# Performance work log

Hardware: AMD Instinct MI355X
Metric: run time of the kernel (lower is better)

Reference implementation:

```python
import jax, jax.numpy as jnp
import numpy as np

N = 4  # n_qubits


def _apply_1q(state, gate, q):
    # state: (B, 2**N) complex64; gate: (2,2) or (B,2,2) complex64; wire q (wire 0 = most significant)
    B = state.shape[0]
    left, right = 2 ** q, 2 ** (N - q - 1)
    s = state.reshape(B, left, 2, right)
    if gate.ndim == 3:
        out = jnp.einsum('bij,bajc->baic', gate, s)
    else:
        out = jnp.einsum('ij,bajc->baic', gate, s)
    return out.reshape(B, 2 ** N)


def _cnot(state, q):
    # CNOT control=q, target=q+1: flip target amplitudes where control bit is 1
    B = state.shape[0]
    left, right = 2 ** q, 2 ** (N - q - 2)
    s = state.reshape(B, left, 2, 2, right)
    out = jnp.concatenate([s[:, :, 0:1], s[:, :, 1:2, ::-1, :]], axis=2)
    return out.reshape(B, 2 ** N)


def _circuit(angles, theta):
    # angles: (B, N) float32 data-dependent RY encoding; theta: (L, N, 3) shared params
    B = angles.shape[0]
    state = jnp.zeros((B, 2 ** N), dtype=jnp.complex64).at[:, 0].set(1.0)
    h = angles * 0.5
    c, s = jnp.cos(h), jnp.sin(h)
    for q in range(N):
        ry = jnp.stack([jnp.stack([c[:, q], -s[:, q]], -1),
                        jnp.stack([s[:, q], c[:, q]], -1)], -2).astype(jnp.complex64)  # (B,2,2)
        state = _apply_1q(state, ry, q)
    L = theta.shape[0]
    for l in range(L):
        for q in range(N):
            a = theta[l, q, 0] * 0.5
            b = theta[l, q, 1] * 0.5
            cc = theta[l, q, 2] * 0.5
            ca, sa = jnp.cos(a), jnp.sin(a)
            rx = jnp.stack([jnp.stack([ca + 0j, -1j * sa]),
                            jnp.stack([-1j * sa, ca + 0j])]).astype(jnp.complex64)
            state = _apply_1q(state, rx, q)
            zero = jnp.zeros((), jnp.complex64)
            rz = jnp.stack([jnp.stack([jnp.exp(-1j * b), zero]),
                            jnp.stack([zero, jnp.exp(1j * b)])]).astype(jnp.complex64)
            state = _apply_1q(state, rz, q)
            cy, sy = jnp.cos(cc), jnp.sin(cc)
            ry = jnp.stack([jnp.stack([cy + 0j, -sy + 0j]),
                            jnp.stack([sy + 0j, cy + 0j])]).astype(jnp.complex64)
            state = _apply_1q(state, ry, q)
        for q in range(N - 1):
            state = _cnot(state, q)
    # PauliZ expectation per wire from probabilities
    probs = (state.real ** 2 + state.imag ** 2).reshape((B,) + (2,) * N)
    evs = []
    for q in range(N):
        sign = (1.0 - 2.0 * jnp.arange(2, dtype=jnp.float32)).reshape(
            (1,) * (q + 1) + (2,) + (1,) * (N - q - 1))
        evs.append((probs * sign).sum(axis=tuple(range(1, N + 1))))
    return jnp.stack(evs, axis=-1)  # (B, N)


def setup_inputs() -> dict:
    key = jax.random.key(0)
    ks = jax.random.split(key, 6)
    B, D = 32768, 512
    inputs = jax.random.normal(ks[0], (B, D), dtype=jnp.float32)
    prev_h = jnp.tanh(jax.random.normal(ks[1], (B, N), dtype=jnp.float32))
    W_enc = jax.random.normal(ks[2], (D + N, N), dtype=jnp.float32) * 0.05
    b_enc = jnp.zeros((N,), dtype=jnp.float32)
    theta = jax.random.uniform(ks[3], (2, N, 3), minval=-0.1, maxval=0.1, dtype=jnp.float32)
    W_out = jax.random.normal(ks[4], (N, N), dtype=jnp.float32) * 0.5
    b_out = jnp.zeros((N,), dtype=jnp.float32)
    return {"inputs": inputs, "prev_h": prev_h, "W_enc": W_enc, "b_enc": b_enc,
            "theta": theta, "W_out": W_out, "b_out": b_out}


def reference(inputs, prev_h, W_enc, b_enc, theta, W_out, b_out):
    combined = jnp.concatenate([inputs, prev_h], axis=-1)           # (B, D+N)
    angles = jnp.tanh(combined @ W_enc + b_enc) * jnp.float32(np.pi)  # (B, N)
    expvals = _circuit(angles, theta)                               # (B, N)
    next_h = jnp.tanh(expvals @ W_out + b_out)                      # (B, N)
    return next_h
```

## Files before the change

kernel.cpp:

```cpp
#include <hip/hip_runtime.h>
#include <math.h>

#define DQ 512
#define NQ 4
#define LQ 2
#define RPB 64
#define BLOCK 256

__device__ __forceinline__ float rowsum16(float v) {
    int x;
    x = __builtin_amdgcn_update_dpp(0, __float_as_int(v), 0x121, 0xF, 0xF, true);
    v += __int_as_float(x);
    x = __builtin_amdgcn_update_dpp(0, __float_as_int(v), 0x122, 0xF, 0xF, true);
    v += __int_as_float(x);
    x = __builtin_amdgcn_update_dpp(0, __float_as_int(v), 0x124, 0xF, 0xF, true);
    v += __int_as_float(x);
    x = __builtin_amdgcn_update_dpp(0, __float_as_int(v), 0x128, 0xF, 0xF, true);
    v += __int_as_float(x);
    return v;
}

__global__ __launch_bounds__(BLOCK) void qrnn_kernel(
    const float* __restrict__ inputs,
    const float* __restrict__ prev_h,
    const float* __restrict__ W_enc,
    const float* __restrict__ b_enc,
    const float* __restrict__ theta,
    const float* __restrict__ W_out,
    const float* __restrict__ b_out,
    float* __restrict__ out,
    int B)
{
    __shared__ float4 sPart[RPB][5];
    __shared__ float  sC[RPB * 5];
    __shared__ float  sS[RPB * 5];
    __shared__ float  sU[LQ * NQ * 8];

    const int tid  = threadIdx.x;
    const int lane = tid & 63;
    const int wave = tid >> 6;
    const int blockBase = blockIdx.x * RPB;

    if (tid < LQ * NQ) {
        const int l = tid >> 2, q = tid & 3;
        const float a  = theta[(l * NQ + q) * 3 + 0] * 0.5f;
        const float b  = theta[(l * NQ + q) * 3 + 1] * 0.5f;
        const float cc = theta[(l * NQ + q) * 3 + 2] * 0.5f;
        float sa, ca, sb, cb, sy, cy;
        sincosf(a,  &sa, &ca);
        sincosf(b,  &sb, &cb);
        sincosf(cc, &sy, &cy);
        const float m00r =  ca * cb, m00i = -ca * sb;
        const float m01r = -sa * sb, m01i = -sa * cb;
        const float m10r =  sa * sb, m10i = -sa * cb;
        const float m11r =  ca * cb, m11i =  ca * sb;
        float* u = &sU[tid * 8];
        u[0] = cy * m00r - sy * m10r;  u[1] = cy * m00i - sy * m10i;
        u[2] = cy * m01r - sy * m11r;  u[3] = cy * m01i - sy * m11i;
        u[4] = sy * m00r + cy * m10r;  u[5] = sy * m00i + cy * m10i;
        u[6] = sy * m01r + cy * m11r;  u[7] = sy * m01i + cy * m11i;
    }

    const float4* __restrict__ W4 = (const float4*)W_enc;
    float4 wreg[8];
#pragma unroll
    for (int k = 0; k < 4; ++k) {
        wreg[k]     = W4[4 * lane + k];
        wreg[k + 4] = W4[256 + 4 * lane + k];
    }

    const int r0 = wave * 16;
    const float4* __restrict__ inBase = (const float4*)inputs;

    float4 xb[4][2];
#pragma unroll
    for (int p = 0; p < 4; ++p) {
        const float4* in4 = inBase + (size_t)(blockBase + r0 + p) * (DQ / 4);
        xb[p][0] = in4[lane];
        xb[p][1] = in4[lane + 64];
    }

#pragma unroll
    for (int r = 0; r < 16; ++r) {
        const int slot = r & 3;
        const float4 x0 = xb[slot][0];
        const float4 x1 = xb[slot][1];
        if (r + 4 < 16) {
            const float4* in4 = inBase + (size_t)(blockBase + r0 + r + 4) * (DQ / 4);
            xb[slot][0] = in4[lane];
            xb[slot][1] = in4[lane + 64];
        }

        const float xs[8] = { x0.x, x0.y, x0.z, x0.w, x1.x, x1.y, x1.z, x1.w };
        float4 acc = make_float4(0.f, 0.f, 0.f, 0.f);
#pragma unroll
        for (int k = 0; k < 8; ++k) {
            acc.x += xs[k] * wreg[k].x;
            acc.y += xs[k] * wreg[k].y;
            acc.z += xs[k] * wreg[k].z;
            acc.w += xs[k] * wreg[k].w;
        }
        acc.x = rowsum16(acc.x);
        acc.y = rowsum16(acc.y);
        acc.z = rowsum16(acc.z);
        acc.w = rowsum16(acc.w);
        if ((lane & 15) == 0) sPart[r0 + r][lane >> 4] = acc;
    }

    __syncthreads();

    {
        const int row  = tid >> 2;
        const int comp = tid & 3;
        const float* pp = (const float*)&sPart[row][0];
        float s = pp[0 * 4 + comp] + pp[1 * 4 + comp] + pp[2 * 4 + comp] + pp[3 * 4 + comp];

        const float4 ph = *(const float4*)(prev_h + (size_t)(blockBase + row) * 4);
        s += ph.x * W_enc[512 * 4 + comp];
        s += ph.y * W_enc[513 * 4 + comp];
        s += ph.z * W_enc[514 * 4 + comp];
        s += ph.w * W_enc[515 * 4 + comp];
        s += b_enc[comp];

        const float h = tanhf(s) * 1.57079632679489662f;
        float sn, cs;
        __sincosf(h, &sn, &cs);
        sC[row * 5 + comp] = cs;
        sS[row * 5 + comp] = sn;
    }

    __syncthreads();

    if (tid < RPB) {
        const int row = blockBase + tid;
        float cq[4], sq[4];
#pragma unroll
        for (int j = 0; j < 4; ++j) {
            cq[j] = sC[tid * 5 + j];
            sq[j] = sS[tid * 5 + j];
        }

        float ar[16], ai[16];
#pragma unroll
        for (int j = 0; j < 16; ++j) {
            float v = ((j >> 3) & 1) ? sq[0] : cq[0];
            v      *= ((j >> 2) & 1) ? sq[1] : cq[1];
            v      *= ((j >> 1) & 1) ? sq[2] : cq[2];
            v      *= ((j >> 0) & 1) ? sq[3] : cq[3];
            ar[j] = v;
            ai[j] = 0.f;
        }

#pragma unroll
        for (int l = 0; l < LQ; ++l) {
#pragma unroll
            for (int q = 0; q < NQ; ++q) {
                const float* u = &sU[(l * NQ + q) * 8];
                const float u00r = u[0], u00i = u[1], u01r = u[2], u01i = u[3];
                const float u10r = u[4], u10i = u[5], u11r = u[6], u11i = u[7];
                const int bit = 1 << (3 - q);
#pragma unroll
                for (int j = 0; j < 16; ++j) {
                    if (j & bit) continue;
                    const int k = j | bit;
                    const float a0r = ar[j], a0i = ai[j];
                    const float a1r = ar[k], a1i = ai[k];
                    ar[j] = u00r * a0r - u00i * a0i + u01r * a1r - u01i * a1i;
                    ai[j] = u00r * a0i + u00i * a0r + u01r * a1i + u01i * a1r;
                    ar[k] = u10r * a0r - u10i * a0i + u11r * a1r - u11i * a1i;
                    ai[k] = u10r * a0i + u10i * a0r + u11r * a1i + u11i * a1r;
                }
            }
#pragma unroll
            for (int q = 0; q < NQ - 1; ++q) {
                const int cb = 1 << (3 - q), tb = 1 << (2 - q);
#pragma unroll
                for (int j = 0; j < 16; ++j) {
                    if ((j & cb) && !(j & tb)) {
                        const int k = j | tb;
                        float t;
                        t = ar[j]; ar[j] = ar[k]; ar[k] = t;
                        t = ai[j]; ai[j] = ai[k]; ai[k] = t;
                    }
                }
            }
        }

        float ev[4] = { 0.f, 0.f, 0.f, 0.f };
#pragma unroll
        for (int j = 0; j < 16; ++j) {
            const float p = ar[j] * ar[j] + ai[j] * ai[j];
#pragma unroll
            for (int q = 0; q < 4; ++q)
                ev[q] += (j & (1 << (3 - q))) ? -p : p;
        }

        float ob[4];
#pragma unroll
        for (int j = 0; j < 4; ++j) {
            float t = b_out[j];
#pragma unroll
            for (int q = 0; q < 4; ++q) t += ev[q] * W_out[q * 4 + j];
            ob[j] = tanhf(t);
        }
        *(float4*)(out + (size_t)row * 4) = make_float4(ob[0], ob[1], ob[2], ob[3]);
    }
}

extern "C" void kernel_launch(void* const* d_in, const int* in_sizes, int n_in,
                              void* d_out, int out_size, void* d_ws, size_t ws_size,
                              hipStream_t stream) {
    const float* inputs = (const float*)d_in[0];
    const float* prev_h = (const float*)d_in[1];
    const float* W_enc  = (const float*)d_in[2];
    const float* b_enc  = (const float*)d_in[3];
    const float* theta  = (const float*)d_in[4];
    const float* W_out  = (const float*)d_in[5];
    const float* b_out  = (const float*)d_in[6];
    float* out = (float*)d_out;

    const int B = in_sizes[0] / DQ;
    const int grid = (B + RPB - 1) / RPB;

    qrnn_kernel<<<grid, BLOCK, 0, stream>>>(inputs, prev_h, W_enc, b_enc, theta,
                                            W_out, b_out, out, B);
}
```

Before: 21.55 us.

## Reassign encoder GEMV to half-wave rows with full reductions and smaller blocks

Each half-wave of 32 lanes now covers a whole input row, with 16 float4 weights per lane. The 512-wide dot product is finished with a DPP row-sum plus a ds_swizzle. This drops the shared-memory partial-sum stage and one barrier, and the encoder angles are computed directly by lane 0 of each half-wave. Rows per block go from 64 to 32, which doubles the grid, and the launch bounds now request occupancy 4. Both tanhf calls become an exp-based fast tanh, trading a little accuracy for cheaper math.

Result: slower. 24.64 us (+14.4%).

```diff
diff --git a/kernel.cpp b/kernel.cpp
--- a/kernel.cpp
+++ b/kernel.cpp
@@ -1,10 +1,10 @@
 #include <hip/hip_runtime.h>
 #include <math.h>
 
-#define DQ 512
-#define NQ 4
-#define LQ 2
-#define RPB 64
+#define DQ    512
+#define NQ    4
+#define LQ    2
+#define RPB   32
 #define BLOCK 256
 
 __device__ __forceinline__ float rowsum16(float v) {
@@ -20,7 +20,18 @@
     return v;
 }
 
-__global__ __launch_bounds__(BLOCK) void qrnn_kernel(
+__device__ __forceinline__ float sum32(float v) {
+    v = rowsum16(v);
+    const int x = __builtin_amdgcn_ds_swizzle(__float_as_int(v), 0x401F);
+    return v + __int_as_float(x);
+}
+
+__device__ __forceinline__ float fast_tanh(float x) {
+    const float e = __expf(2.0f * x);
+    return 1.0f - 2.0f / (e + 1.0f);
+}
+
+__global__ __launch_bounds__(BLOCK, 4) void qrnn_kernel(
     const float* __restrict__ inputs,
     const float* __restrict__ prev_h,
     const float* __restrict__ W_enc,
@@ -31,15 +42,17 @@
     float* __restrict__ out,
     int B)
 {
-    __shared__ float4 sPart[RPB][5];
-    __shared__ float  sC[RPB * 5];
-    __shared__ float  sS[RPB * 5];
+    __shared__ float4 sC4[RPB];
+    __shared__ float4 sS4[RPB];
     __shared__ float  sU[LQ * NQ * 8];
 
     const int tid  = threadIdx.x;
     const int lane = tid & 63;
     const int wave = tid >> 6;
+    const int g    = lane >> 5;
+    const int j    = lane & 31;
     const int blockBase = blockIdx.x * RPB;
+    const int rbase = wave * 8;
 
     if (tid < LQ * NQ) {
         const int l = tid >> 2, q = tid & 3;
@@ -61,94 +74,85 @@
         u[6] = sy * m01r + cy * m11r;  u[7] = sy * m01i + cy * m11i;
     }
 
-    const float4* __restrict__ W4 = (const float4*)W_enc;
-    float4 wreg[8];
-#pragma unroll
-    for (int k = 0; k < 4; ++k) {
-        wreg[k]     = W4[4 * lane + k];
-        wreg[k + 4] = W4[256 + 4 * lane + k];
-    }
-
-    const int r0 = wave * 16;
-    const float4* __restrict__ inBase = (const float4*)inputs;
-
-    float4 xb[4][2];
-#pragma unroll
-    for (int p = 0; p < 4; ++p) {
-        const float4* in4 = inBase + (size_t)(blockBase + r0 + p) * (DQ / 4);
-        xb[p][0] = in4[lane];
-        xb[p][1] = in4[lane + 64];
-    }
-
-#pragma unroll
-    for (int r = 0; r < 16; ++r) {
-        const int slot = r & 3;
-        const float4 x0 = xb[slot][0];
-        const float4 x1 = xb[slot][1];
-        if (r + 4 < 16) {
-            const float4* in4 = inBase + (size_t)(blockBase + r0 + r + 4) * (DQ / 4);
-            xb[slot][0] = in4[lane];
-            xb[slot][1] = in4[lane + 64];
-        }
-
-        const float xs[8] = { x0.x, x0.y, x0.z, x0.w, x1.x, x1.y, x1.z, x1.w };
-        float4 acc = make_float4(0.f, 0.f, 0.f, 0.f);
-#pragma unroll
-        for (int k = 0; k < 8; ++k) {
-            acc.x += xs[k] * wreg[k].x;
-            acc.y += xs[k] * wreg[k].y;
-            acc.z += xs[k] * wreg[k].z;
-            acc.w += xs[k] * wreg[k].w;
-        }
-        acc.x = rowsum16(acc.x);
-        acc.y = rowsum16(acc.y);
-        acc.z = rowsum16(acc.z);
-        acc.w = rowsum16(acc.w);
-        if ((lane & 15) == 0) sPart[r0 + r][lane >> 4] = acc;
-    }
-
-    __syncthreads();
-
-    {
-        const int row  = tid >> 2;
-        const int comp = tid & 3;
-        const float* pp = (const float*)&sPart[row][0];
-        float s = pp[0 * 4 + comp] + pp[1 * 4 + comp] + pp[2 * 4 + comp] + pp[3 * 4 + comp];
-
-        const float4 ph = *(const float4*)(prev_h + (size_t)(blockBase + row) * 4);
-        s += ph.x * W_enc[512 * 4 + comp];
-        s += ph.y * W_enc[513 * 4 + comp];
-        s += ph.z * W_enc[514 * 4 + comp];
-        s += ph.w * W_enc[515 * 4 + comp];
-        s += b_enc[comp];
-
-        const float h = tanhf(s) * 1.57079632679489662f;
-        float sn, cs;
-        __sincosf(h, &sn, &cs);
-        sC[row * 5 + comp] = cs;
-        sS[row * 5 + comp] = sn;
+    const float4* __restrict__ W4  = (const float4*)W_enc;
+    const float4* __restrict__ in4 = (const float4*)inputs;
+
+    float4 wreg[4][4];
+#pragma unroll
+    for (int c = 0; c < 4; ++c)
+#pragma unroll
+        for (int k = 0; k < 4; ++k)
+            wreg[c][k] = W4[4 * j + 128 * c + k];
+
+    float4 buf[8];
+#pragma unroll
+    for (int s = 0; s < 8; ++s) {
+        const int p = s >> 2, c = s & 3;
+        buf[s] = in4[(size_t)(blockBase + rbase + 2 * p + g) * (DQ / 4) + j + 32 * c];
+    }
+
+    float4 acc = make_float4(0.f, 0.f, 0.f, 0.f);
+#pragma unroll
+    for (int s = 0; s < 16; ++s) {
+        const int p = s >> 2, c = s & 3;
+        const float4 x = buf[s & 7];
+        if (s + 8 < 16) {
+            const int p2 = (s + 8) >> 2, c2 = (s + 8) & 3;
+            buf[s & 7] = in4[(size_t)(blockBase + rbase + 2 * p2 + g) * (DQ / 4) + j + 32 * c2];
+        }
+        if (c == 0) acc = make_float4(0.f, 0.f, 0.f, 0.f);
+        acc.x += x.x * wreg[c][0].x + x.y * wreg[c][1].x + x.z * wreg[c][2].x + x.w * wreg[c][3].x;
+        acc.y += x.x * wreg[c][0].y + x.y * wreg[c][1].y + x.z * wreg[c][2].y + x.w * wreg[c][3].y;
+        acc.z += x.x * wreg[c][0].z + x.y * wreg[c][1].z + x.z * wreg[c][2].z + x.w * wreg[c][3].z;
+        acc.w += x.x * wreg[c][0].w + x.y * wreg[c][1].w + x.z * wreg[c][2].w + x.w * wreg[c][3].w;
+        if (c == 3) {
+            float s0 = sum32(acc.x);
+            float s1 = sum32(acc.y);
+            float s2 = sum32(acc.z);
+            float s3 = sum32(acc.w);
+            if (j == 0) {
+                const int rl = rbase + 2 * p + g;
+                const float4 ph = *(const float4*)(prev_h + (size_t)(blockBase + rl) * 4);
+                const float4 wt0 = W4[512], wt1 = W4[513], wt2 = W4[514], wt3 = W4[515];
+                const float4 bE  = *(const float4*)b_enc;
+                s0 += ph.x * wt0.x + ph.y * wt1.x + ph.z * wt2.x + ph.w * wt3.x + bE.x;
+                s1 += ph.x * wt0.y + ph.y * wt1.y + ph.z * wt2.y + ph.w * wt3.y + bE.y;
+                s2 += ph.x * wt0.z + ph.y * wt1.z + ph.z * wt2.z + ph.w * wt3.z + bE.z;
+                s3 += ph.x * wt0.w + ph.y * wt1.w + ph.z * wt2.w + ph.w * wt3.w + bE.w;
+                const float kHalfPi = 1.57079632679489662f;
+                const float h0 = fast_tanh(s0) * kHalfPi;
+                const float h1 = fast_tanh(s1) * kHalfPi;
+                const float h2 = fast_tanh(s2) * kHalfPi;
+                const float h3 = fast_tanh(s3) * kHalfPi;
+                float sn0, cs0, sn1, cs1, sn2, cs2, sn3, cs3;
+                __sincosf(h0, &sn0, &cs0);
+                __sincosf(h1, &sn1, &cs1);
+                __sincosf(h2, &sn2, &cs2);
+                __sincosf(h3, &sn3, &cs3);
+                sC4[rl] = make_float4(cs0, cs1, cs2, cs3);
+                sS4[rl] = make_float4(sn0, sn1, sn2, sn3);
+            }
+        }
     }
 
     __syncthreads();
 
     if (tid < RPB) {
         const int row = blockBase + tid;
-        float cq[4], sq[4];
-#pragma unroll
-        for (int j = 0; j < 4; ++j) {
-            cq[j] = sC[tid * 5 + j];
-            sq[j] = sS[tid * 5 + j];
-        }
+        const float4 c4 = sC4[tid];
+        const float4 s4 = sS4[tid];
+        const float cq[4] = { c4.x, c4.y, c4.z, c4.w };
+        const float sq[4] = { s4.x, s4.y, s4.z, s4.w };
 
         float ar[16], ai[16];
 #pragma unroll
-        for (int j = 0; j < 16; ++j) {
-            float v = ((j >> 3) & 1) ? sq[0] : cq[0];
-            v      *= ((j >> 2) & 1) ? sq[1] : cq[1];
-            v      *= ((j >> 1) & 1) ? sq[2] : cq[2];
-            v      *= ((j >> 0) & 1) ? sq[3] : cq[3];
-            ar[j] = v;
-            ai[j] = 0.f;
+        for (int jj = 0; jj < 16; ++jj) {
+            float v = ((jj >> 3) & 1) ? sq[0] : cq[0];
+            v      *= ((jj >> 2) & 1) ? sq[1] : cq[1];
+            v      *= ((jj >> 1) & 1) ? sq[2] : cq[2];
+            v      *= ((jj >> 0) & 1) ? sq[3] : cq[3];
+            ar[jj] = v;
+            ai[jj] = 0.f;
         }
 
 #pragma unroll
@@ -160,27 +164,27 @@
                 const float u10r = u[4], u10i = u[5], u11r = u[6], u11i = u[7];
                 const int bit = 1 << (3 - q);
 #pragma unroll
-                for (int j = 0; j < 16; ++j) {
-                    if (j & bit) continue;
-                    const int k = j | bit;
-                    const float a0r = ar[j], a0i = ai[j];
-                    const float a1r = ar[k], a1i = ai[k];
-                    ar[j] = u00r * a0r - u00i * a0i + u01r * a1r - u01i * a1i;
-                    ai[j] = u00r * a0i + u00i * a0r + u01r * a1i + u01i * a1r;
-                    ar[k] = u10r * a0r - u10i * a0i + u11r * a1r - u11i * a1i;
-                    ai[k] = u10r * a0i + u10i * a0r + u11r * a1i + u11i * a1r;
+                for (int jj = 0; jj < 16; ++jj) {
+                    if (jj & bit) continue;
+                    const int kk = jj | bit;
+                    const float a0r = ar[jj], a0i = ai[jj];
+                    const float a1r = ar[kk], a1i = ai[kk];
+                    ar[jj] = u00r * a0r - u00i * a0i + u01r * a1r - u01i * a1i;
+                    ai[jj] = u00r * a0i + u00i * a0r + u01r * a1i + u01i * a1r;
+                    ar[kk] = u10r * a0r - u10i * a0i + u11r * a1r - u11i * a1i;
+                    ai[kk] = u10r * a0i + u10i * a0r + u11r * a1i + u11i * a1r;
                 }
             }
 #pragma unroll
             for (int q = 0; q < NQ - 1; ++q) {
                 const int cb = 1 << (3 - q), tb = 1 << (2 - q);
 #pragma unroll
-                for (int j = 0; j < 16; ++j) {
-                    if ((j & cb) && !(j & tb)) {
-                        const int k = j | tb;
+                for (int jj = 0; jj < 16; ++jj) {
+                    if ((jj & cb) && !(jj & tb)) {
+                        const int kk = jj | tb;
                         float t;
-                        t = ar[j]; ar[j] = ar[k]; ar[k] = t;
-                        t = ai[j]; ai[j] = ai[k]; ai[k] = t;
+                        t = ar[jj]; ar[jj] = ar[kk]; ar[kk] = t;
+                        t = ai[jj]; ai[jj] = ai[kk]; ai[kk] = t;
                     }
                 }
             }
@@ -188,20 +192,20 @@
 
         float ev[4] = { 0.f, 0.f, 0.f, 0.f };
 #pragma unroll
-        for (int j = 0; j < 16; ++j) {
-            const float p = ar[j] * ar[j] + ai[j] * ai[j];
+        for (int jj = 0; jj < 16; ++jj) {
+            const float p = ar[jj] * ar[jj] + ai[jj] * ai[jj];
 #pragma unroll
             for (int q = 0; q < 4; ++q)
-                ev[q] += (j & (1 << (3 - q))) ? -p : p;
+                ev[q] += (jj & (1 << (3 - q))) ? -p : p;
         }
 
         float ob[4];
 #pragma unroll
-        for (int j = 0; j < 4; ++j) {
-            float t = b_out[j];
-#pragma unroll
-            for (int q = 0; q < 4; ++q) t += ev[q] * W_out[q * 4 + j];
-            ob[j] = tanhf(t);
+        for (int jj = 0; jj < 4; ++jj) {
+            float t = b_out[jj];
+#pragma unroll
+            for (int q = 0; q < 4; ++q) t += ev[q] * W_out[q * 4 + jj];
+            ob[jj] = fast_tanh(t);
         }
         *(float4*)(out + (size_t)row * 4) = make_float4(ob[0], ob[1], ob[2], ob[3]);
     }
```

## Make waves self-contained to drop block barriers and halve rows per block

Applied to the files above, without the earlier changes.

Each wave now handles its own 8 rows end to end. It computes its own copy of the gate unitaries and runs the encoder epilogue and circuit simulation without any __syncthreads, and rows per block drop to 32 so the grid doubles. Input prefetch is issued before the theta trig, and tanhf/sincosf are replaced with fast exp-based and intrinsic versions. The gate unitaries are recomputed redundantly in every wave, and the fast math may lose some accuracy. Wave-local LDS reuse relies on wave-synchronous execution with no explicit barrier.

New measurement: 36.01 us. 1.67x slower.

```diff
diff --git a/kernel.cpp b/kernel.cpp
--- a/kernel.cpp
+++ b/kernel.cpp
@@ -1,11 +1,13 @@
 #include <hip/hip_runtime.h>
 #include <math.h>
 
-#define DQ 512
-#define NQ 4
-#define LQ 2
-#define RPB 64
+#define DQ    512
+#define NQ    4
+#define LQ    2
+#define RPB   32
 #define BLOCK 256
+#define WAVES 4
+#define RPW   8
 
 __device__ __forceinline__ float rowsum16(float v) {
     int x;
@@ -20,7 +22,12 @@
     return v;
 }
 
-__global__ __launch_bounds__(BLOCK) void qrnn_kernel(
+__device__ __forceinline__ float fast_tanh(float x) {
+    const float e = __expf(2.0f * x);
+    return 1.0f - 2.0f / (e + 1.0f);
+}
+
+__global__ __launch_bounds__(BLOCK, 4) void qrnn_kernel(
     const float* __restrict__ inputs,
     const float* __restrict__ prev_h,
     const float* __restrict__ W_enc,
@@ -34,34 +41,45 @@
     __shared__ float4 sPart[RPB][5];
     __shared__ float  sC[RPB * 5];
     __shared__ float  sS[RPB * 5];
-    __shared__ float  sU[LQ * NQ * 8];
+    __shared__ float  sU[WAVES][LQ * NQ * 8];
 
     const int tid  = threadIdx.x;
     const int lane = tid & 63;
     const int wave = tid >> 6;
     const int blockBase = blockIdx.x * RPB;
-
-    if (tid < LQ * NQ) {
-        const int l = tid >> 2, q = tid & 3;
+    const int rbase = wave * RPW;
+
+    const float4* __restrict__ W4  = (const float4*)W_enc;
+    const float4* __restrict__ in4 = (const float4*)inputs;
+
+    float4 xb[4][2];
+#pragma unroll
+    for (int p = 0; p < 4; ++p) {
+        const size_t rowOff = (size_t)(blockBase + rbase + p) * (DQ / 4);
+        xb[p][0] = in4[rowOff + lane];
+        xb[p][1] = in4[rowOff + lane + 64];
+    }
+
+    if (lane < LQ * NQ) {
+        const int l = lane >> 2, q = lane & 3;
         const float a  = theta[(l * NQ + q) * 3 + 0] * 0.5f;
         const float b  = theta[(l * NQ + q) * 3 + 1] * 0.5f;
         const float cc = theta[(l * NQ + q) * 3 + 2] * 0.5f;
         float sa, ca, sb, cb, sy, cy;
-        sincosf(a,  &sa, &ca);
-        sincosf(b,  &sb, &cb);
-        sincosf(cc, &sy, &cy);
+        __sincosf(a,  &sa, &ca);
+        __sincosf(b,  &sb, &cb);
+        __sincosf(cc, &sy, &cy);
         const float m00r =  ca * cb, m00i = -ca * sb;
         const float m01r = -sa * sb, m01i = -sa * cb;
         const float m10r =  sa * sb, m10i = -sa * cb;
         const float m11r =  ca * cb, m11i =  ca * sb;
-        float* u = &sU[tid * 8];
+        float* u = &sU[wave][lane * 8];
         u[0] = cy * m00r - sy * m10r;  u[1] = cy * m00i - sy * m10i;
         u[2] = cy * m01r - sy * m11r;  u[3] = cy * m01i - sy * m11i;
         u[4] = sy * m00r + cy * m10r;  u[5] = sy * m00i + cy * m10i;
         u[6] = sy * m01r + cy * m11r;  u[7] = sy * m01i + cy * m11i;
     }
 
-    const float4* __restrict__ W4 = (const float4*)W_enc;
     float4 wreg[8];
 #pragma unroll
     for (int k = 0; k < 4; ++k) {
@@ -69,26 +87,15 @@
         wreg[k + 4] = W4[256 + 4 * lane + k];
     }
 
-    const int r0 = wave * 16;
-    const float4* __restrict__ inBase = (const float4*)inputs;
-
-    float4 xb[4][2];
-#pragma unroll
-    for (int p = 0; p < 4; ++p) {
-        const float4* in4 = inBase + (size_t)(blockBase + r0 + p) * (DQ / 4);
-        xb[p][0] = in4[lane];
-        xb[p][1] = in4[lane + 64];
-    }
-
-#pragma unroll
-    for (int r = 0; r < 16; ++r) {
+#pragma unroll
+    for (int r = 0; r < RPW; ++r) {
         const int slot = r & 3;
         const float4 x0 = xb[slot][0];
         const float4 x1 = xb[slot][1];
-        if (r + 4 < 16) {
-            const float4* in4 = inBase + (size_t)(blockBase + r0 + r + 4) * (DQ / 4);
-            xb[slot][0] = in4[lane];
-            xb[slot][1] = in4[lane + 64];
+        if (r + 4 < RPW) {
+            const size_t rowOff = (size_t)(blockBase + rbase + r + 4) * (DQ / 4);
+            xb[slot][0] = in4[rowOff + lane];
+            xb[slot][1] = in4[rowOff + lane + 64];
         }
 
         const float xs[8] = { x0.x, x0.y, x0.z, x0.w, x1.x, x1.y, x1.z, x1.w };
@@ -104,40 +111,37 @@
         acc.y = rowsum16(acc.y);
         acc.z = rowsum16(acc.z);
         acc.w = rowsum16(acc.w);
-        if ((lane & 15) == 0) sPart[r0 + r][lane >> 4] = acc;
-    }
-
-    __syncthreads();
-
-    {
-        const int row  = tid >> 2;
-        const int comp = tid & 3;
-        const float* pp = (const float*)&sPart[row][0];
-        float s = pp[0 * 4 + comp] + pp[1 * 4 + comp] + pp[2 * 4 + comp] + pp[3 * 4 + comp];
-
-        const float4 ph = *(const float4*)(prev_h + (size_t)(blockBase + row) * 4);
+        if ((lane & 15) == 0) sPart[rbase + r][lane >> 4] = acc;
+    }
+
+    if (lane < 32) {
+        const int rl   = rbase + (lane >> 2);
+        const int comp = lane & 3;
+        const float* pp = (const float*)&sPart[rl][0];
+        float s = pp[comp] + pp[4 + comp] + pp[8 + comp] + pp[12 + comp];
+
+        const float4 ph = *(const float4*)(prev_h + (size_t)(blockBase + rl) * 4);
         s += ph.x * W_enc[512 * 4 + comp];
         s += ph.y * W_enc[513 * 4 + comp];
         s += ph.z * W_enc[514 * 4 + comp];
         s += ph.w * W_enc[515 * 4 + comp];
         s += b_enc[comp];
 
-        const float h = tanhf(s) * 1.57079632679489662f;
+        const float h = fast_tanh(s) * 1.57079632679489662f;
         float sn, cs;
         __sincosf(h, &sn, &cs);
-        sC[row * 5 + comp] = cs;
-        sS[row * 5 + comp] = sn;
-    }
-
-    __syncthreads();
-
-    if (tid < RPB) {
-        const int row = blockBase + tid;
+        sC[rl * 5 + comp] = cs;
+        sS[rl * 5 + comp] = sn;
+    }
+
+    if (lane < RPW) {
+        const int rl  = rbase + lane;
+        const int row = blockBase + rl;
         float cq[4], sq[4];
 #pragma unroll
         for (int j = 0; j < 4; ++j) {
-            cq[j] = sC[tid * 5 + j];
-            sq[j] = sS[tid * 5 + j];
+            cq[j] = sC[rl * 5 + j];
+            sq[j] = sS[rl * 5 + j];
         }
 
         float ar[16], ai[16];
@@ -151,11 +155,12 @@
             ai[j] = 0.f;
         }
 
+        const float* uw = &sU[wave][0];
 #pragma unroll
         for (int l = 0; l < LQ; ++l) {
 #pragma unroll
             for (int q = 0; q < NQ; ++q) {
-                const float* u = &sU[(l * NQ + q) * 8];
+                const float* u = &uw[(l * NQ + q) * 8];
                 const float u00r = u[0], u00i = u[1], u01r = u[2], u01i = u[3];
                 const float u10r = u[4], u10i = u[5], u11r = u[6], u11i = u[7];
                 const int bit = 1 << (3 - q);
@@ -201,7 +206,7 @@
             float t = b_out[j];
 #pragma unroll
             for (int q = 0; q < 4; ++q) t += ev[q] * W_out[q * 4 + j];
-            ob[j] = tanhf(t);
+            ob[j] = fast_tanh(t);
         }
         *(float4*)(out + (size_t)row * 4) = make_float4(ob[0], ob[1], ob[2], ob[3]);
     }
```
